# Optimization experiments

Measured on AMD Instinct MI355X. Metric: run time of the kernel, lower is better.

The kernel has to match this reference:

```python
import jax, jax.numpy as jnp
import numpy as np

B, T, C, H = 8, 1024, 768, 12
D = C // H  # head_dim = 64


def setup_inputs() -> dict:
    key = jax.random.key(0)
    ks = jax.random.split(key, 6)
    s = 1.0 / np.sqrt(C)
    x = jax.random.normal(ks[0], (B, T, C), dtype=jnp.float32)
    Wq = jax.random.normal(ks[1], (C, C), dtype=jnp.float32) * s
    Wk = jax.random.normal(ks[2], (C, C), dtype=jnp.float32) * s
    Wv = jax.random.normal(ks[3], (C, C), dtype=jnp.float32) * s
    Wo = jax.random.normal(ks[4], (C, C), dtype=jnp.float32) * s
    bq = jnp.zeros((C,), jnp.float32)
    bk = jnp.zeros((C,), jnp.float32)
    bv = jnp.zeros((C,), jnp.float32)
    bo = jnp.zeros((C,), jnp.float32)
    # causal mask, broadcastable to [B, H, T, T]
    mask = jnp.tril(jnp.ones((T, T), dtype=bool))[None, None, :, :]
    return {"x": x, "mask": mask, "Wq": Wq, "bq": bq, "Wk": Wk, "bk": bk,
            "Wv": Wv, "bv": bv, "Wo": Wo, "bo": bo}


def reference(x, mask, Wq, bq, Wk, bk, Wv, bv, Wo, bo):
    # QKV projections: [B,T,C] @ [C,C] -> [B,T,C]
    q = x @ Wq + bq
    k = x @ Wk + bk
    v = x @ Wv + bv
    # split heads -> [B,H,T,D]
    q = q.reshape(B, T, H, D).transpose(0, 2, 1, 3)
    k = k.reshape(B, T, H, D).transpose(0, 2, 1, 3)
    v = v.reshape(B, T, H, D).transpose(0, 2, 1, 3)
    scale = 1.0 / jnp.sqrt(jnp.float32(D))
    scores = jnp.einsum('bhtd,bhsd->bhts', q, k) * scale  # [B,H,T,T]
    scores = jnp.where(mask, scores, jnp.float32(-1e9))
    attn = jax.nn.softmax(scores, axis=-1)
    out = jnp.einsum('bhts,bhsd->bhtd', attn, v)  # [B,H,T,D]
    out = out.transpose(0, 2, 1, 3).reshape(B, T, C)
    return out @ Wo + bo
```

## Files before the change

### kernel.cpp

```cpp
#include <hip/hip_runtime.h>
#include <hip/hip_bf16.h>

#define B 8
#define T 1024
#define C 768
#define H 12
#define D 64
#define M (B * T)

typedef unsigned short u16;
typedef unsigned int u32;
typedef __attribute__((ext_vector_type(8))) short bf16x8;
typedef __attribute__((ext_vector_type(4))) float f32x4;

__device__ __forceinline__ u16 f2bf(float f) {
  union { float f; u32 u; } c; c.f = f;
  u32 r = c.u + 0x7FFF + ((c.u >> 16) & 1);
  return (u16)(r >> 16);
}

__device__ __forceinline__ void gload16(const void* g, void* l) {
  __builtin_amdgcn_global_load_lds(
      (const __attribute__((address_space(1))) void*)g,
      (__attribute__((address_space(3))) void*)l, 16, 0, 0);
}

__device__ __forceinline__ int swzA(int row) {
  return (row & 3) ^ ((row >> 2) & 1);
}

__global__ __launch_bounds__(256) void prep_kernel(
    const float* __restrict__ x,
    const float* __restrict__ Wq, const float* __restrict__ Wk,
    const float* __restrict__ Wv, const float* __restrict__ Wo,
    u16* __restrict__ xb, u16* __restrict__ WtQKV, u16* __restrict__ WoT) {
  __shared__ float t[32][33];
  const int bx = blockIdx.x;
  if (bx < 2048) {
    const int n4 = M * C / 4;
    for (int i = bx * 256 + threadIdx.x; i < n4; i += 2048 * 256) {
      float4 v = ((const float4*)x)[i];
      ushort4 o;
      o.x = f2bf(v.x); o.y = f2bf(v.y); o.z = f2bf(v.z); o.w = f2bf(v.w);
      ((ushort4*)xb)[i] = o;
    }
    return;
  }
  const int i = bx - 2048;
  const int z = i / 576;
  const int rem = i % 576;
  const int k0 = (rem / 24) * 32, n0 = (rem % 24) * 32;
  const float* W = (z == 0) ? Wq : (z == 1) ? Wk : (z == 2) ? Wv : Wo;
  u16* dst = (z < 3) ? (WtQKV + (size_t)z * 768 * 768) : WoT;
  const int tx = threadIdx.x & 31, ty = threadIdx.x >> 5;
#pragma unroll
  for (int j = 0; j < 4; j++) {
    int r = ty * 4 + j;
    t[r][tx] = W[(size_t)(k0 + r) * 768 + n0 + tx];
  }
  __syncthreads();
#pragma unroll
  for (int j = 0; j < 4; j++) {
    int r = ty * 4 + j;
    dst[(size_t)(n0 + r) * 768 + k0 + tx] = f2bf(t[tx][r]);
  }
}

template <typename OutT, bool ROWBIAS, int BN>
__global__ __launch_bounds__(256) void gemm_mfma_kernel(
    const u16* __restrict__ A,
    const u16* __restrict__ Wt,
    const float* __restrict__ b0, const float* __restrict__ b1,
    OutT* __restrict__ o0, OutT* __restrict__ o1,
    int ldOut, float sc0, float sc1) {
  constexpr int NJ = BN / 32;
  constexpr int BT = BN * 4 / 256;
  __shared__ u16 As[128 * 32];
  __shared__ u16 Bs[BN * 32];
  const int tid = threadIdx.x;
  const int w = tid >> 6, l = tid & 63;
  const int g = l >> 4, c = l & 15;
  const int m0 = blockIdx.y * 128;
  const int n0g = blockIdx.x * BN;
  const int seg = (!ROWBIAS && n0g >= 768) ? 1 : 0;
  const int n0 = n0g - seg * 768;
  const float* bias = (seg == 0) ? b0 : b1;
  OutT* out = (seg == 0) ? o0 : o1;
  const float sc = (seg == 0) ? sc0 : sc1;
  const int wr = (w >> 1) * 64, wc = (w & 1) * (BN / 2);

  f32x4 acc[4][NJ];
#pragma unroll
  for (int i = 0; i < 4; i++)
#pragma unroll
    for (int j = 0; j < NJ; j++) acc[i][j] = f32x4{0.f, 0.f, 0.f, 0.f};

  for (int k0 = 0; k0 < 768; k0 += 32) {
    __syncthreads();
#pragma unroll
    for (int t = 0; t < 2; t++) {
      int ii = w * 2 + t;
      int e16 = ii * 64 + l;
      int row = e16 >> 2, slot = e16 & 3;
      int gs = slot ^ swzA(row);
      gload16(A + (size_t)(m0 + row) * 768 + k0 + gs * 8, (char*)As + ii * 1024);
    }
#pragma unroll
    for (int t = 0; t < BT; t++) {
      int ii = w * BT + t;
      int e16 = ii * 64 + l;
      int row = e16 >> 2, slot = e16 & 3;
      int gs = slot ^ swzA(row);
      gload16(Wt + (size_t)(n0g + row) * 768 + k0 + gs * 8, (char*)Bs + ii * 1024);
    }
    __syncthreads();

    bf16x8 af[4], bfr[NJ];
#pragma unroll
    for (int i = 0; i < 4; i++) {
      int row = wr + i * 16 + c;
      int slot = g ^ swzA(row);
      af[i] = *(const bf16x8*)(As + row * 32 + slot * 8);
    }
#pragma unroll
    for (int j = 0; j < NJ; j++) {
      int row = wc + j * 16 + c;
      int slot = g ^ swzA(row);
      bfr[j] = *(const bf16x8*)(Bs + row * 32 + slot * 8);
    }
#pragma unroll
    for (int i = 0; i < 4; i++)
#pragma unroll
      for (int j = 0; j < NJ; j++)
        acc[i][j] = __builtin_amdgcn_mfma_f32_16x16x32_bf16(af[i], bfr[j], acc[i][j], 0, 0, 0);
  }

  float brow[4][4];
  if (ROWBIAS) {
#pragma unroll
    for (int i = 0; i < 4; i++)
#pragma unroll
      for (int r = 0; r < 4; r++)
        brow[i][r] = b0[m0 + wr + i * 16 + g * 4 + r];
  }
#pragma unroll
  for (int j = 0; j < NJ; j++) {
    int col = n0 + wc + j * 16 + c;
    float bcol = ROWBIAS ? 0.f : bias[col];
#pragma unroll
    for (int i = 0; i < 4; i++) {
#pragma unroll
      for (int r = 0; r < 4; r++) {
        int row = m0 + wr + i * 16 + g * 4 + r;
        float v = (acc[i][j][r] + (ROWBIAS ? brow[i][r] : bcol)) * sc;
        if constexpr (sizeof(OutT) == 2) {
          ((u16*)out)[(size_t)row * ldOut + col] = f2bf(v);
        } else {
          ((float*)out)[(size_t)row * ldOut + col] = v;
        }
      }
    }
  }
}

__global__ __launch_bounds__(256) void attn_mfma_kernel(
    const u16* __restrict__ Qb, const u16* __restrict__ Kb,
    const u16* __restrict__ VT, u16* __restrict__ Ob) {
  __shared__ u16 Ks[128 * 64];
  __shared__ u16 Vs[64 * 128];
  __shared__ u16 Ps[4][16][132];

  const int tid = threadIdx.x;
  const int w = tid >> 6, l = tid & 63;
  const int g = l >> 4, c = l & 15;

  const int wg = blockIdx.x;
  const int logical = (wg & 7) * 192 + (wg >> 3);
  const int bh = logical >> 4;
  const int qi = 15 - (logical & 15);
  const int q0 = qi * 64;
  const int b = bh / H, h = bh % H;
  const int qw = q0 + w * 16;

  bf16x8 qf[2];
  {
    size_t base = (size_t)(b * T + qw + c) * C + h * D;
    qf[0] = *(const bf16x8*)(Qb + base + g * 8);
    qf[1] = *(const bf16x8*)(Qb + base + 32 + g * 8);
  }

  f32x4 acc[4];
#pragma unroll
  for (int j = 0; j < 4; j++) acc[j] = f32x4{0.f, 0.f, 0.f, 0.f};
  float m_i[4], l_p[4];
#pragma unroll
  for (int r = 0; r < 4; r++) { m_i[r] = -1e30f; l_p[r] = 0.f; }

  const int nt = q0 / 128 + 1;
  for (int it = 0; it < nt; it++) {
    const int s0 = it * 128;
    __syncthreads();
#pragma unroll
    for (int t = 0; t < 4; t++) {
      int ii = w * 4 + t;
      int e16 = ii * 64 + l;
      int row = e16 >> 3, slot = e16 & 7;
      int gs = slot ^ (row & 7);
      gload16(Kb + (size_t)(b * T + s0 + row) * C + h * D + gs * 8, (char*)Ks + ii * 1024);
    }
#pragma unroll
    for (int t = 0; t < 4; t++) {
      int ii = w * 4 + t;
      int e16 = ii * 64 + l;
      int row = e16 >> 4, slot = e16 & 15;
      int gs = slot ^ (row & 15);
      gload16(VT + (size_t)(h * D + row) * M + b * T + s0 + gs * 8, (char*)Vs + ii * 1024);
    }
    __syncthreads();

    const bool active = (s0 <= qw + 15);
    if (active) {
      f32x4 s[8];
#pragma unroll
      for (int f = 0; f < 8; f++) s[f] = f32x4{0.f, 0.f, 0.f, 0.f};
      __builtin_amdgcn_s_setprio(1);
#pragma unroll
      for (int f = 0; f < 8; f++) {
        int kvrow = f * 16 + c;
#pragma unroll
        for (int kc = 0; kc < 2; kc++) {
          int slot = (kc * 4 + g) ^ (kvrow & 7);
          bf16x8 kf = *(const bf16x8*)(Ks + kvrow * 64 + slot * 8);
          s[f] = __builtin_amdgcn_mfma_f32_16x16x32_bf16(qf[kc], kf, s[f], 0, 0, 0);
        }
      }
      __builtin_amdgcn_s_setprio(0);
      const bool partial = (s0 + 127 > qw);
      if (partial) {
#pragma unroll
        for (int r = 0; r < 4; r++) {
          int q = qw + g * 4 + r;
#pragma unroll
          for (int f = 0; f < 8; f++) {
            int kv = s0 + f * 16 + c;
            if (kv > q) s[f][r] = -1e30f;
          }
        }
      }
      float mx[4];
#pragma unroll
      for (int r = 0; r < 4; r++) {
        float mr = s[0][r];
#pragma unroll
        for (int f = 1; f < 8; f++) mr = fmaxf(mr, s[f][r]);
        mx[r] = mr;
      }
#pragma unroll
      for (int off = 1; off < 16; off <<= 1)
#pragma unroll
        for (int r = 0; r < 4; r++) mx[r] = fmaxf(mx[r], __shfl_xor(mx[r], off, 64));
      bool defer = true;
#pragma unroll
      for (int r = 0; r < 4; r++) defer = defer && (mx[r] <= m_i[r] + 8.0f);
      if (!__all(defer)) {
#pragma unroll
        for (int r = 0; r < 4; r++) {
          float mn = fmaxf(m_i[r], mx[r]);
          float rc = exp2f(m_i[r] - mn);
          m_i[r] = mn;
          l_p[r] *= rc;
#pragma unroll
          for (int j = 0; j < 4; j++) acc[j][r] *= rc;
        }
      }
#pragma unroll
      for (int r = 0; r < 4; r++) {
        float sum = 0.f;
#pragma unroll
        for (int f = 0; f < 8; f++) {
          float p = exp2f(s[f][r] - m_i[r]);
          s[f][r] = p;
          sum += p;
        }
        l_p[r] += sum;
#pragma unroll
        for (int f = 0; f < 8; f += 2) {
          __hip_bfloat162 h2 = __float22bfloat162_rn(make_float2(s[f][r], s[f + 1][r]));
          u32 pk = *(u32*)&h2;
          Ps[w][g * 4 + r][f * 16 + c] = (u16)pk;
          Ps[w][g * 4 + r][(f + 1) * 16 + c] = (u16)(pk >> 16);
        }
      }
      __builtin_amdgcn_s_setprio(1);
#pragma unroll
      for (int kc = 0; kc < 4; kc++) {
        bf16x8 pf = *(const bf16x8*)(&Ps[w][c][kc * 32 + g * 8]);
#pragma unroll
        for (int j = 0; j < 4; j++) {
          bf16x8 vf = *(const bf16x8*)(Vs + (j * 16 + c) * 128 + (((kc * 4 + g) ^ c) * 8));
          acc[j] = __builtin_amdgcn_mfma_f32_16x16x32_bf16(pf, vf, acc[j], 0, 0, 0);
        }
      }
      __builtin_amdgcn_s_setprio(0);
    }
  }

  float inv[4];
#pragma unroll
  for (int r = 0; r < 4; r++) {
    float v = l_p[r];
#pragma unroll
    for (int off = 1; off < 16; off <<= 1) v += __shfl_xor(v, off, 64);
    inv[r] = 1.f / v;
  }
#pragma unroll
  for (int j = 0; j < 4; j++) {
#pragma unroll
    for (int r = 0; r < 4; r++) {
      int row = qw + g * 4 + r;
      int col = j * 16 + c;
      Ob[(size_t)(b * T + row) * C + h * D + col] = f2bf(acc[j][r] * inv[r]);
    }
  }
}

extern "C" void kernel_launch(void* const* d_in, const int* in_sizes, int n_in,
                              void* d_out, int out_size, void* d_ws, size_t ws_size,
                              hipStream_t stream) {
  const float* x  = (const float*)d_in[0];
  const float* Wq = (const float*)d_in[2];
  const float* bq = (const float*)d_in[3];
  const float* Wk = (const float*)d_in[4];
  const float* bk = (const float*)d_in[5];
  const float* Wv = (const float*)d_in[6];
  const float* bv = (const float*)d_in[7];
  const float* Wo = (const float*)d_in[8];
  const float* bo = (const float*)d_in[9];
  float* out = (float*)d_out;

  const size_t MC2 = (size_t)M * C * 2;
  char* ws = (char*)d_ws;
  u16* xb    = (u16*)(ws);
  u16* WtQKV = (u16*)(ws + MC2);
  u16* WoT   = (u16*)(ws + MC2 + 3538944);
  u16* Qb    = (u16*)(ws + MC2 + 3538944 + 1179648);
  u16* Kb    = (u16*)((char*)Qb + MC2);
  u16* VT    = (u16*)((char*)Kb + MC2);
  u16* Ob    = (u16*)((char*)VT + MC2);
  u16* WvT   = WtQKV + 2 * 768 * 768;

  const float qscale = 0.125f * 1.4426950408889634f;

  prep_kernel<<<4352, 256, 0, stream>>>(x, Wq, Wk, Wv, Wo, xb, WtQKV, WoT);
  gemm_mfma_kernel<u16, false, 128><<<dim3(12, 64), 256, 0, stream>>>(
      xb, WtQKV, bq, bk, Qb, Kb, 768, qscale, 1.f);
  gemm_mfma_kernel<u16, true, 128><<<dim3(64, 6), 256, 0, stream>>>(
      WvT, xb, bv, bv, VT, VT, M, 1.f, 1.f);
  attn_mfma_kernel<<<1536, 256, 0, stream>>>(Qb, Kb, VT, Ob);
  gemm_mfma_kernel<float, false, 128><<<dim3(6, 64), 256, 0, stream>>>(
      Ob, WoT, bo, bo, out, out, 768, 1.f, 1.f);
}
```

Before: 137.1 us.

## Load V fragments directly from global in attention; XCD-swizzle GEMM block mapping

The attention kernel stops staging V^T tiles in shared memory and instead reads each bf16x8 V fragment straight from global memory inside the PV MFMA loop. This removes the V LDS fill and its footprint, but every wave now issues its own global loads of V with the latency exposed in the inner loop. Separately, the GEMM kernel switches to a 1D grid with a round-robin remapping of block IDs across 8 groups, apparently meant to place neighbouring tiles on the same XCD for better L2 reuse.

```diff
diff --git a/kernel.cpp b/kernel.cpp
--- a/kernel.cpp
+++ b/kernel.cpp
@@ -66,34 +66,34 @@
   }
 }
 
-template <typename OutT, bool ROWBIAS, int BN>
+template <typename OutT, bool ROWBIAS, int NBCOLS>
 __global__ __launch_bounds__(256) void gemm_mfma_kernel(
     const u16* __restrict__ A,
     const u16* __restrict__ Wt,
     const float* __restrict__ b0, const float* __restrict__ b1,
     OutT* __restrict__ o0, OutT* __restrict__ o1,
     int ldOut, float sc0, float sc1) {
-  constexpr int NJ = BN / 32;
-  constexpr int BT = BN * 4 / 256;
   __shared__ u16 As[128 * 32];
-  __shared__ u16 Bs[BN * 32];
+  __shared__ u16 Bs[128 * 32];
   const int tid = threadIdx.x;
   const int w = tid >> 6, l = tid & 63;
   const int g = l >> 4, c = l & 15;
-  const int m0 = blockIdx.y * 128;
-  const int n0g = blockIdx.x * BN;
+  const int nwg8 = gridDim.x >> 3;
+  const int swz = (blockIdx.x & 7) * nwg8 + (blockIdx.x >> 3);
+  const int m0 = (swz / NBCOLS) * 128;
+  const int n0g = (swz % NBCOLS) * 128;
   const int seg = (!ROWBIAS && n0g >= 768) ? 1 : 0;
   const int n0 = n0g - seg * 768;
   const float* bias = (seg == 0) ? b0 : b1;
   OutT* out = (seg == 0) ? o0 : o1;
   const float sc = (seg == 0) ? sc0 : sc1;
-  const int wr = (w >> 1) * 64, wc = (w & 1) * (BN / 2);
-
-  f32x4 acc[4][NJ];
+  const int wr = (w >> 1) * 64, wc = (w & 1) * 64;
+
+  f32x4 acc[4][4];
 #pragma unroll
   for (int i = 0; i < 4; i++)
 #pragma unroll
-    for (int j = 0; j < NJ; j++) acc[i][j] = f32x4{0.f, 0.f, 0.f, 0.f};
+    for (int j = 0; j < 4; j++) acc[i][j] = f32x4{0.f, 0.f, 0.f, 0.f};
 
   for (int k0 = 0; k0 < 768; k0 += 32) {
     __syncthreads();
@@ -106,8 +106,8 @@
       gload16(A + (size_t)(m0 + row) * 768 + k0 + gs * 8, (char*)As + ii * 1024);
     }
 #pragma unroll
-    for (int t = 0; t < BT; t++) {
-      int ii = w * BT + t;
+    for (int t = 0; t < 2; t++) {
+      int ii = w * 2 + t;
       int e16 = ii * 64 + l;
       int row = e16 >> 2, slot = e16 & 3;
       int gs = slot ^ swzA(row);
@@ -115,7 +115,7 @@
     }
     __syncthreads();
 
-    bf16x8 af[4], bfr[NJ];
+    bf16x8 af[4], bfr[4];
 #pragma unroll
     for (int i = 0; i < 4; i++) {
       int row = wr + i * 16 + c;
@@ -123,7 +123,7 @@
       af[i] = *(const bf16x8*)(As + row * 32 + slot * 8);
     }
 #pragma unroll
-    for (int j = 0; j < NJ; j++) {
+    for (int j = 0; j < 4; j++) {
       int row = wc + j * 16 + c;
       int slot = g ^ swzA(row);
       bfr[j] = *(const bf16x8*)(Bs + row * 32 + slot * 8);
@@ -131,7 +131,7 @@
 #pragma unroll
     for (int i = 0; i < 4; i++)
 #pragma unroll
-      for (int j = 0; j < NJ; j++)
+      for (int j = 0; j < 4; j++)
         acc[i][j] = __builtin_amdgcn_mfma_f32_16x16x32_bf16(af[i], bfr[j], acc[i][j], 0, 0, 0);
   }
 
@@ -144,7 +144,7 @@
         brow[i][r] = b0[m0 + wr + i * 16 + g * 4 + r];
   }
 #pragma unroll
-  for (int j = 0; j < NJ; j++) {
+  for (int j = 0; j < 4; j++) {
     int col = n0 + wc + j * 16 + c;
     float bcol = ROWBIAS ? 0.f : bias[col];
 #pragma unroll
@@ -167,7 +167,6 @@
     const u16* __restrict__ Qb, const u16* __restrict__ Kb,
     const u16* __restrict__ VT, u16* __restrict__ Ob) {
   __shared__ u16 Ks[128 * 64];
-  __shared__ u16 Vs[64 * 128];
   __shared__ u16 Ps[4][16][132];
 
   const int tid = threadIdx.x;
@@ -189,6 +188,8 @@
     qf[1] = *(const bf16x8*)(Qb + base + 32 + g * 8);
   }
 
+  const u16* vbh = VT + (size_t)h * D * M + (size_t)b * T;
+
   f32x4 acc[4];
 #pragma unroll
   for (int j = 0; j < 4; j++) acc[j] = f32x4{0.f, 0.f, 0.f, 0.f};
@@ -208,14 +209,6 @@
       int gs = slot ^ (row & 7);
       gload16(Kb + (size_t)(b * T + s0 + row) * C + h * D + gs * 8, (char*)Ks + ii * 1024);
     }
-#pragma unroll
-    for (int t = 0; t < 4; t++) {
-      int ii = w * 4 + t;
-      int e16 = ii * 64 + l;
-      int row = e16 >> 4, slot = e16 & 15;
-      int gs = slot ^ (row & 15);
-      gload16(VT + (size_t)(h * D + row) * M + b * T + s0 + gs * 8, (char*)Vs + ii * 1024);
-    }
     __syncthreads();
 
     const bool active = (s0 <= qw + 15);
@@ -297,7 +290,8 @@
         bf16x8 pf = *(const bf16x8*)(&Ps[w][c][kc * 32 + g * 8]);
 #pragma unroll
         for (int j = 0; j < 4; j++) {
-          bf16x8 vf = *(const bf16x8*)(Vs + (j * 16 + c) * 128 + (((kc * 4 + g) ^ c) * 8));
+          bf16x8 vf = *(const bf16x8*)(
+              vbh + (size_t)(j * 16 + c) * M + s0 + kc * 32 + g * 8);
           acc[j] = __builtin_amdgcn_mfma_f32_16x16x32_bf16(pf, vf, acc[j], 0, 0, 0);
         }
       }
@@ -352,11 +346,11 @@
   const float qscale = 0.125f * 1.4426950408889634f;
 
   prep_kernel<<<4352, 256, 0, stream>>>(x, Wq, Wk, Wv, Wo, xb, WtQKV, WoT);
-  gemm_mfma_kernel<u16, false, 128><<<dim3(12, 64), 256, 0, stream>>>(
+  gemm_mfma_kernel<u16, false, 12><<<768, 256, 0, stream>>>(
       xb, WtQKV, bq, bk, Qb, Kb, 768, qscale, 1.f);
-  gemm_mfma_kernel<u16, true, 128><<<dim3(64, 6), 256, 0, stream>>>(
+  gemm_mfma_kernel<u16, true, 64><<<384, 256, 0, stream>>>(
       WvT, xb, bv, bv, VT, VT, M, 1.f, 1.f);
   attn_mfma_kernel<<<1536, 256, 0, stream>>>(Qb, Kb, VT, Ob);
-  gemm_mfma_kernel<float, false, 128><<<dim3(6, 64), 256, 0, stream>>>(
+  gemm_mfma_kernel<float, false, 6><<<384, 256, 0, stream>>>(
       Ob, WoT, bo, bo, out, out, 768, 1.f, 1.f);
 }
```

Result: slower. 172.5 us (+25.9%).
